# Optimization experiments

Hardware: AMD Instinct MI355X
Metric: run time of the kernel (lower is better)

The kernel has to match this reference:

```python
import jax, jax.numpy as jnp
import numpy as np

TOP_K = 50
TAU = 0.02
EPS = 1e-12  # torch F.normalize eps


def setup_inputs() -> dict:
    key = jax.random.key(0)
    k1, k2 = jax.random.split(key)
    test_patches = jax.random.normal(k1, (2048, 256), dtype=jnp.float32)
    memory_nodes_gpu = jax.random.normal(k2, (100000, 256), dtype=jnp.float32)
    return {"test_patches": test_patches, "memory_nodes_gpu": memory_nodes_gpu}


def _l2norm(x):
    n = jnp.linalg.norm(x, axis=-1, keepdims=True)
    return x / jnp.maximum(n, EPS)


def reference(test_patches, memory_nodes_gpu):
    # [P, M] similarity
    sim = jnp.matmul(test_patches, memory_nodes_gpu.T)
    K = min(TOP_K, memory_nodes_gpu.shape[0])
    topk_sim, topk_idx = jax.lax.top_k(sim, K)          # [P, K]
    attn = jax.nn.softmax(topk_sim / TAU, axis=1)        # [P, K]
    gathered = memory_nodes_gpu[topk_idx]                # [P, K, D]
    messages = jnp.einsum('pk,pkd->pd', attn, gathered)  # [P, D]
    updated = _l2norm(test_patches + messages)           # [P, D]
    evidence = topk_sim[:, 0]                            # [P]
    ew = jax.nn.softmax(evidence / TAU)[:, None]          # [P, 1]
    global_feature = jnp.sum(updated * ew, axis=0, keepdims=True)  # [1, D]
    return _l2norm(global_feature), updated
```

## Files before the change

kernel.cpp:

```cpp
#include <hip/hip_runtime.h>
#include <cstdint>
#include <cstddef>

#define NP      2048
#define NN      100000
#define DIM     256
#define NT      6250
#define NG      1563
#define NG2     3126
#define NG2R    3125
#define NGT2    3328
#define NTP     (NG * 4)
#define CPX     25
#define INV_TAU 50.0f
#define MARGIN  0.7f
#define CUT     0.553f
#define LCAP    64

typedef __fp16 half8  __attribute__((ext_vector_type(8)));
typedef __fp16 half2v __attribute__((ext_vector_type(2)));
typedef float  floatx4 __attribute__((ext_vector_type(4)));

union H8 { half8 v8; half2v v2[4]; };

typedef const __attribute__((address_space(1))) char* gptr_t;
typedef __attribute__((address_space(3))) char* sptr_t;

__device__ __forceinline__ unsigned enc_f32(float f) {
    unsigned b = __float_as_uint(f);
    return (b & 0x80000000u) ? ~b : (b | 0x80000000u);
}
__device__ __forceinline__ float dec_f32(unsigned u) {
    unsigned b = (u & 0x80000000u) ? (u & 0x7FFFFFFFu) : ~u;
    return __uint_as_float(b);
}

__global__ __launch_bounds__(512)
void k_convB(const float* __restrict__ B, __fp16* __restrict__ Bh,
             unsigned* __restrict__ me_u)
{
    const int t    = (int)blockIdx.x;
    const int ks   = (int)threadIdx.x >> 6;
    const int lane = (int)threadIdx.x & 63;
    if (t == 0 && threadIdx.x == 0) me_u[0] = 0u;
    H8 h;
    if (t < NT) {
        const int node = t * 16 + (lane & 15);
        const int d0   = ((lane >> 4) << 3) + (ks << 5);
        const float* bp = B + (size_t)node * DIM + d0;
        float4 b0 = *reinterpret_cast<const float4*>(bp);
        float4 b1 = *reinterpret_cast<const float4*>(bp + 4);
        h.v2[0] = __builtin_amdgcn_cvt_pkrtz(b0.x, b0.y);
        h.v2[1] = __builtin_amdgcn_cvt_pkrtz(b0.z, b0.w);
        h.v2[2] = __builtin_amdgcn_cvt_pkrtz(b1.x, b1.y);
        h.v2[3] = __builtin_amdgcn_cvt_pkrtz(b1.z, b1.w);
    } else {
        h.v2[0] = __builtin_amdgcn_cvt_pkrtz(0.f, 0.f);
        h.v2[1] = h.v2[0]; h.v2[2] = h.v2[0]; h.v2[3] = h.v2[0];
    }
    *reinterpret_cast<half8*>(Bh + (((size_t)t * 8 + ks) * 64 + lane) * 8) = h.v8;
}

__global__ __launch_bounds__(256, 2)
void k_pass1(const float* __restrict__ A, const __fp16* __restrict__ Bh,
             float* __restrict__ tmax2)
{
    __shared__ __fp16 lds[2][16384];

    const int tid  = (int)threadIdx.x;
    const int w    = tid >> 6;
    const int lane = tid & 63;
    const int col  = lane & 15;
    const int kg   = lane >> 4;

    const int bid   = (int)blockIdx.x;
    const int chunk = (bid & 7) * 8 + ((bid >> 3) & 7);
    const int rb    = bid >> 6;

    const int g0 = chunk * CPX;
    if (g0 >= NG) return;
    const int g1 = (g0 + CPX < NG) ? g0 + CPX : NG;
    const int wrow0 = rb * 256 + w * 64;

    H8 af[4][8];
#pragma unroll
    for (int rs = 0; rs < 4; ++rs) {
        const float* ap = A + (size_t)(wrow0 + rs * 16 + col) * DIM + (kg << 3);
#pragma unroll
        for (int ks = 0; ks < 8; ++ks) {
            float4 x0 = *reinterpret_cast<const float4*>(ap + (ks << 5));
            float4 x1 = *reinterpret_cast<const float4*>(ap + (ks << 5) + 4);
            af[rs][ks].v2[0] = __builtin_amdgcn_cvt_pkrtz(x0.x, x0.y);
            af[rs][ks].v2[1] = __builtin_amdgcn_cvt_pkrtz(x0.z, x0.w);
            af[rs][ks].v2[2] = __builtin_amdgcn_cvt_pkrtz(x1.x, x1.y);
            af[rs][ks].v2[3] = __builtin_amdgcn_cvt_pkrtz(x1.z, x1.w);
        }
    }

    auto STAGE = [&](int buf, int g) {
        const char* src = (const char*)Bh + ((size_t)g << 15) + (w << 13) + (lane << 4);
        char* dstb = (char*)&lds[buf][0] + (w << 13);
#pragma unroll
        for (int i = 0; i < 8; ++i)
            __builtin_amdgcn_global_load_lds((gptr_t)(src + (i << 10)),
                                             (sptr_t)(dstb + (i << 10)), 16, 0, 0);
    };

    STAGE(0, g0);
    int cur = 0;
    for (int g = g0; g < g1; ++g) {
        asm volatile("s_waitcnt vmcnt(0)" ::: "memory");
        __syncthreads();
        if (g + 1 < g1) STAGE(cur ^ 1, g + 1);

        const __fp16* base = &lds[cur][0] + lane * 8;
        float tmh[2][4];
#pragma unroll
        for (int hh = 0; hh < 2; ++hh)
#pragma unroll
            for (int rs = 0; rs < 4; ++rs) tmh[hh][rs] = -INFINITY;

        half8 bfA[8], bfB[8];
#pragma unroll
        for (int ks = 0; ks < 8; ++ks)
            bfA[ks] = *reinterpret_cast<const half8*>(base + ks * 512);

        auto FMI = [&](half8 (&curf)[8], half8 (&nxtf)[8], int ttn, bool ld, int hh) {
            floatx4 acc[4];
#pragma unroll
            for (int rs = 0; rs < 4; ++rs) acc[rs] = (floatx4){0.f, 0.f, 0.f, 0.f};
#pragma unroll
            for (int ks = 0; ks < 8; ++ks) {
                if (ld)
                    nxtf[ks] = *reinterpret_cast<const half8*>(base + ttn * 4096 + ks * 512);
                acc[0] = __builtin_amdgcn_mfma_f32_16x16x32_f16(curf[ks], af[0][ks].v8, acc[0], 0, 0, 0);
                acc[1] = __builtin_amdgcn_mfma_f32_16x16x32_f16(curf[ks], af[1][ks].v8, acc[1], 0, 0, 0);
                acc[2] = __builtin_amdgcn_mfma_f32_16x16x32_f16(curf[ks], af[2][ks].v8, acc[2], 0, 0, 0);
                acc[3] = __builtin_amdgcn_mfma_f32_16x16x32_f16(curf[ks], af[3][ks].v8, acc[3], 0, 0, 0);
            }
#pragma unroll
            for (int rs = 0; rs < 4; ++rs)
                tmh[hh][rs] = fmaxf(tmh[hh][rs], fmaxf(fmaxf(acc[rs][0], acc[rs][1]),
                                                       fmaxf(acc[rs][2], acc[rs][3])));
        };

        FMI(bfA, bfB, 1, true,  0);
        FMI(bfB, bfA, 2, true,  0);
        FMI(bfA, bfB, 3, true,  1);
        FMI(bfB, bfA, 0, false, 1);

#pragma unroll
        for (int hh = 0; hh < 2; ++hh)
#pragma unroll
            for (int rs = 0; rs < 4; ++rs) {
                tmh[hh][rs] = fmaxf(tmh[hh][rs], __shfl_xor(tmh[hh][rs], 16));
                tmh[hh][rs] = fmaxf(tmh[hh][rs], __shfl_xor(tmh[hh][rs], 32));
            }
        if (kg == 0) {
#pragma unroll
            for (int hh = 0; hh < 2; ++hh)
#pragma unroll
                for (int rs = 0; rs < 4; ++rs)
                    tmax2[(size_t)(g * 2 + hh) * NP + wrow0 + rs * 16 + col] = tmh[hh][rs];
        }
        cur ^= 1;
    }
}

__global__ __launch_bounds__(256)
void k_tr(const float* __restrict__ tmax2, float* __restrict__ tmaxT)
{
    __shared__ float tile[64][65];
    const int t  = (int)threadIdx.x;
    const int g0 = (int)blockIdx.x * 64;
    const int r0 = (int)blockIdx.y * 64;
    const int a  = t & 63;
    const int b  = t >> 6;
#pragma unroll
    for (int it = 0; it < 16; ++it) {
        int gi = b + it * 4;
        int g  = g0 + gi;
        tile[gi][a] = (g < NG2) ? tmax2[(size_t)g * NP + r0 + a] : -INFINITY;
    }
    __syncthreads();
#pragma unroll
    for (int it = 0; it < 16; ++it) {
        int ri = b + it * 4;
        tmaxT[(size_t)(r0 + ri) * NGT2 + g0 + a] = tile[a][ri];
    }
}

__global__ __launch_bounds__(256)
void k_finish(const float* __restrict__ A, const float* __restrict__ B,
              const float* __restrict__ tmaxT, float* __restrict__ out,
              float* __restrict__ evidence, unsigned* __restrict__ me_u)
{
    __shared__ float ald8[8][36];
    __shared__ float sims[32];
    __shared__ float red[8];
    __shared__ int   list[LCAP];
    __shared__ int   wsum[4];

    const int t    = (int)threadIdx.x;
    const int row  = (int)blockIdx.x;
    const int lane = t & 63;
    const int wv   = t >> 6;

    const float av_own = A[(size_t)row * DIM + t];
    ald8[t >> 5][t & 31] = av_own;

    float v[13];
    const float* tr = tmaxT + (size_t)row * NGT2 + t * 13;
    float M = -INFINITY;
#pragma unroll
    for (int k = 0; k < 13; ++k) { v[k] = tr[k]; M = fmaxf(M, v[k]); }
#pragma unroll
    for (int o = 1; o < 64; o <<= 1) M = fmaxf(M, __shfl_xor(M, o));
    if (lane == 0) red[wv] = M;
    __syncthreads();
    M = fmaxf(fmaxf(red[0], red[1]), fmaxf(red[2], red[3]));

    const float thr = M - MARGIN;
    int cnt = 0; unsigned mask13 = 0u;
#pragma unroll
    for (int k = 0; k < 13; ++k)
        if (v[k] > thr && (t * 13 + k) < NG2R) { mask13 |= (1u << k); ++cnt; }
    int pre = cnt;
#pragma unroll
    for (int o = 1; o < 64; o <<= 1) {
        int x = __shfl_up(pre, o);
        if (lane >= o) pre += x;
    }
    if (lane == 63) wsum[wv] = pre;
    __syncthreads();
    int woff = 0;
    for (int i = 0; i < wv; ++i) woff += wsum[i];
    int pos = woff + pre - cnt;
    if (mask13) {
#pragma unroll
        for (int k = 0; k < 13; ++k)
            if (mask13 & (1u << k)) {
                if (pos < LCAP) list[pos] = t * 13 + k;
                ++pos;
            }
    }
    __syncthreads();
    int total = wsum[0] + wsum[1] + wsum[2] + wsum[3];
    if (total > LCAP) total = LCAP;

    float m = -INFINITY, l = 0.f, msg = 0.f;
    const int n = t >> 3, q8 = t & 7;

    for (int e = 0; e < total; ++e) {
        const int g  = list[e];
        const int n0 = g * 32;
        {
            float s = 0.f;
            const float4* bp = reinterpret_cast<const float4*>(B + (size_t)(n0 + n) * DIM + q8 * 32);
            const float4* ap = reinterpret_cast<const float4*>(&ald8[q8][0]);
#pragma unroll
            for (int i = 0; i < 8; ++i) {
                float4 b4 = bp[i], a4 = ap[i];
                s += a4.x * b4.x + a4.y * b4.y + a4.z * b4.z + a4.w * b4.w;
            }
            s += __shfl_xor(s, 1);
            s += __shfl_xor(s, 2);
            s += __shfl_xor(s, 4);
            __syncthreads();
            if (q8 == 0) sims[n] = s;
            __syncthreads();
        }
        float gm = -INFINITY;
#pragma unroll
        for (int i = 0; i < 32; ++i) gm = fmaxf(gm, sims[i]);
        if (gm > m) {
            float sc = __expf((m - gm) * INV_TAU);
            m = gm; l *= sc; msg *= sc;
        }
        const float cut = m - CUT;
        for (int i = 0; i < 32; ++i) {
            float si = sims[i];
            if (si > cut) {
                float wn = __expf((si - m) * INV_TAU);
                l += wn;
                msg += wn * B[(size_t)(n0 + i) * DIM + t];
            }
        }
    }

    float u = av_own + msg * (1.0f / l);
    float ss = u * u;
#pragma unroll
    for (int o = 1; o < 64; o <<= 1) ss += __shfl_xor(ss, o);
    if (lane == 0) red[4 + wv] = ss;
    __syncthreads();
    ss = (red[4] + red[5]) + (red[6] + red[7]);
    float rn = 1.0f / fmaxf(sqrtf(ss), 1e-12f);
    out[256 + (size_t)row * DIM + t] = u * rn;
    if (t == 0) {
        evidence[row] = m;
        atomicMax(me_u, enc_f32(m));
    }
}

__global__ __launch_bounds__(256)
void k_gpart(const float* __restrict__ evidence, const unsigned* __restrict__ me_u,
             const float* __restrict__ out, float* __restrict__ gpart)
{
    __shared__ float wsh[128];
    int tid = (int)threadIdx.x;
    int r0  = blockIdx.x * 128;
    float Me = dec_f32(me_u[0]);
    if (tid < 128) wsh[tid] = __expf((evidence[r0 + tid] - Me) * INV_TAU);
    __syncthreads();
    float g = 0.0f;
    for (int k = 0; k < 128; ++k)
        g += wsh[k] * out[256 + (size_t)(r0 + k) * DIM + tid];
    gpart[blockIdx.x * 256 + tid] = g;
}

__global__ __launch_bounds__(256)
void k_final(const float* __restrict__ gpart, float* __restrict__ out)
{
    __shared__ float red[256];
    int tid = (int)threadIdx.x;
    float g = 0.0f;
#pragma unroll
    for (int b = 0; b < 16; ++b) g += gpart[b * 256 + tid];
    red[tid] = g * g; __syncthreads();
    for (int s = 128; s > 0; s >>= 1) {
        if (tid < s) red[tid] += red[tid + s];
        __syncthreads();
    }
    float n = sqrtf(red[0]);
    float r = 1.0f / fmaxf(n, 1e-12f);
    out[tid] = g * r;
}

extern "C" void kernel_launch(void* const* d_in, const int* in_sizes, int n_in,
                              void* d_out, int out_size, void* d_ws, size_t ws_size,
                              hipStream_t stream)
{
    const float* A = (const float*)d_in[0];
    const float* B = (const float*)d_in[1];
    float* out = (float*)d_out;
    float* ws  = (float*)d_ws;

    __fp16* Bh      = (__fp16*)ws;
    float* tmaxT    = ws;
    float* tmax2    = ws + (size_t)NTP * 2048;
    float* evidence = tmax2 + (size_t)NG2 * NP;
    unsigned* me_u  = (unsigned*)(evidence + NP);
    float* gpart    = (float*)(me_u + 16);

    k_convB <<<NTP,           512, 0, stream>>>(B, Bh, me_u);
    k_pass1 <<<512,           256, 0, stream>>>(A, Bh, tmax2);
    k_tr    <<<dim3(52, 32),  256, 0, stream>>>(tmax2, tmaxT);
    k_finish<<<NP,            256, 0, stream>>>(A, B, tmaxT, out, evidence, me_u);
    k_gpart <<<16,            256, 0, stream>>>(evidence, me_u, out, gpart);
    k_final <<<1,             256, 0, stream>>>(gpart, out);
}
```

Before: 182.6 us.

## Load B fragments directly from global and write transposed tile maxima, dropping transpose kernel

k_pass1 no longer stages B tiles into LDS with global_load_lds and barriers. Each wave now reads its half8 fragments straight from global memory into registers, double-buffered across tile pairs. It writes the per-row group maxima directly in row-major tmaxT layout, so the separate k_tr transpose kernel and its tmax2 buffer are removed. k_finish masks out-of-range entries at load time instead of relying on -inf padding. This trades LDS sharing and coalesced stores for per-wave global reads, which depend on L2 hits, and for strided scattered stores of the maxima.

Result: slower. 186.4 us (+2.1%).

```diff
diff --git a/kernel.cpp b/kernel.cpp
--- a/kernel.cpp
+++ b/kernel.cpp
@@ -7,7 +7,6 @@
 #define DIM     256
 #define NT      6250
 #define NG      1563
-#define NG2     3126
 #define NG2R    3125
 #define NGT2    3328
 #define NTP     (NG * 4)
@@ -22,9 +21,6 @@
 typedef float  floatx4 __attribute__((ext_vector_type(4)));
 
 union H8 { half8 v8; half2v v2[4]; };
-
-typedef const __attribute__((address_space(1))) char* gptr_t;
-typedef __attribute__((address_space(3))) char* sptr_t;
 
 __device__ __forceinline__ unsigned enc_f32(float f) {
     unsigned b = __float_as_uint(f);
@@ -63,10 +59,8 @@
 
 __global__ __launch_bounds__(256, 2)
 void k_pass1(const float* __restrict__ A, const __fp16* __restrict__ Bh,
-             float* __restrict__ tmax2)
-{
-    __shared__ __fp16 lds[2][16384];
-
+             float* __restrict__ tmaxT)
+{
     const int tid  = (int)threadIdx.x;
     const int w    = tid >> 6;
     const int lane = tid & 63;
@@ -97,96 +91,53 @@
         }
     }
 
-    auto STAGE = [&](int buf, int g) {
-        const char* src = (const char*)Bh + ((size_t)g << 15) + (w << 13) + (lane << 4);
-        char* dstb = (char*)&lds[buf][0] + (w << 13);
-#pragma unroll
-        for (int i = 0; i < 8; ++i)
-            __builtin_amdgcn_global_load_lds((gptr_t)(src + (i << 10)),
-                                             (sptr_t)(dstb + (i << 10)), 16, 0, 0);
+    const half8* bbl = reinterpret_cast<const half8*>(Bh) + lane;
+
+    float tm[4];
+    auto LD = [&](half8 (&bf)[8], int tt) {
+#pragma unroll
+        for (int ks = 0; ks < 8; ++ks)
+            bf[ks] = bbl[(size_t)tt * 512 + ks * 64];
     };
-
-    STAGE(0, g0);
-    int cur = 0;
-    for (int g = g0; g < g1; ++g) {
-        asm volatile("s_waitcnt vmcnt(0)" ::: "memory");
-        __syncthreads();
-        if (g + 1 < g1) STAGE(cur ^ 1, g + 1);
-
-        const __fp16* base = &lds[cur][0] + lane * 8;
-        float tmh[2][4];
-#pragma unroll
-        for (int hh = 0; hh < 2; ++hh)
-#pragma unroll
-            for (int rs = 0; rs < 4; ++rs) tmh[hh][rs] = -INFINITY;
-
-        half8 bfA[8], bfB[8];
-#pragma unroll
-        for (int ks = 0; ks < 8; ++ks)
-            bfA[ks] = *reinterpret_cast<const half8*>(base + ks * 512);
-
-        auto FMI = [&](half8 (&curf)[8], half8 (&nxtf)[8], int ttn, bool ld, int hh) {
-            floatx4 acc[4];
-#pragma unroll
-            for (int rs = 0; rs < 4; ++rs) acc[rs] = (floatx4){0.f, 0.f, 0.f, 0.f};
-#pragma unroll
-            for (int ks = 0; ks < 8; ++ks) {
-                if (ld)
-                    nxtf[ks] = *reinterpret_cast<const half8*>(base + ttn * 4096 + ks * 512);
-                acc[0] = __builtin_amdgcn_mfma_f32_16x16x32_f16(curf[ks], af[0][ks].v8, acc[0], 0, 0, 0);
-                acc[1] = __builtin_amdgcn_mfma_f32_16x16x32_f16(curf[ks], af[1][ks].v8, acc[1], 0, 0, 0);
-                acc[2] = __builtin_amdgcn_mfma_f32_16x16x32_f16(curf[ks], af[2][ks].v8, acc[2], 0, 0, 0);
-                acc[3] = __builtin_amdgcn_mfma_f32_16x16x32_f16(curf[ks], af[3][ks].v8, acc[3], 0, 0, 0);
-            }
+    auto FM = [&](const half8 (&bf)[8]) {
+        floatx4 acc[4];
+#pragma unroll
+        for (int rs = 0; rs < 4; ++rs) acc[rs] = (floatx4){0.f, 0.f, 0.f, 0.f};
+#pragma unroll
+        for (int ks = 0; ks < 8; ++ks) {
+            acc[0] = __builtin_amdgcn_mfma_f32_16x16x32_f16(bf[ks], af[0][ks].v8, acc[0], 0, 0, 0);
+            acc[1] = __builtin_amdgcn_mfma_f32_16x16x32_f16(bf[ks], af[1][ks].v8, acc[1], 0, 0, 0);
+            acc[2] = __builtin_amdgcn_mfma_f32_16x16x32_f16(bf[ks], af[2][ks].v8, acc[2], 0, 0, 0);
+            acc[3] = __builtin_amdgcn_mfma_f32_16x16x32_f16(bf[ks], af[3][ks].v8, acc[3], 0, 0, 0);
+        }
+#pragma unroll
+        for (int rs = 0; rs < 4; ++rs)
+            tm[rs] = fmaxf(tm[rs], fmaxf(fmaxf(acc[rs][0], acc[rs][1]),
+                                         fmaxf(acc[rs][2], acc[rs][3])));
+    };
+
+    const int T0 = g0 * 4, T1 = g1 * 4;
+    half8 bf0[8], bf1[8];
+    LD(bf0, T0);
+    for (int t = T0; t < T1; t += 2) {
+        LD(bf1, t + 1);
+        tm[0] = -INFINITY; tm[1] = -INFINITY;
+        tm[2] = -INFINITY; tm[3] = -INFINITY;
+        FM(bf0);
+        if (t + 2 < T1) LD(bf0, t + 2);
+        FM(bf1);
+
+#pragma unroll
+        for (int rs = 0; rs < 4; ++rs) {
+            tm[rs] = fmaxf(tm[rs], __shfl_xor(tm[rs], 16));
+            tm[rs] = fmaxf(tm[rs], __shfl_xor(tm[rs], 32));
+        }
+        if (kg == 0) {
+            const int g2 = t >> 1;
 #pragma unroll
             for (int rs = 0; rs < 4; ++rs)
-                tmh[hh][rs] = fmaxf(tmh[hh][rs], fmaxf(fmaxf(acc[rs][0], acc[rs][1]),
-                                                       fmaxf(acc[rs][2], acc[rs][3])));
-        };
-
-        FMI(bfA, bfB, 1, true,  0);
-        FMI(bfB, bfA, 2, true,  0);
-        FMI(bfA, bfB, 3, true,  1);
-        FMI(bfB, bfA, 0, false, 1);
-
-#pragma unroll
-        for (int hh = 0; hh < 2; ++hh)
-#pragma unroll
-            for (int rs = 0; rs < 4; ++rs) {
-                tmh[hh][rs] = fmaxf(tmh[hh][rs], __shfl_xor(tmh[hh][rs], 16));
-                tmh[hh][rs] = fmaxf(tmh[hh][rs], __shfl_xor(tmh[hh][rs], 32));
-            }
-        if (kg == 0) {
-#pragma unroll
-            for (int hh = 0; hh < 2; ++hh)
-#pragma unroll
-                for (int rs = 0; rs < 4; ++rs)
-                    tmax2[(size_t)(g * 2 + hh) * NP + wrow0 + rs * 16 + col] = tmh[hh][rs];
-        }
-        cur ^= 1;
-    }
-}
-
-__global__ __launch_bounds__(256)
-void k_tr(const float* __restrict__ tmax2, float* __restrict__ tmaxT)
-{
-    __shared__ float tile[64][65];
-    const int t  = (int)threadIdx.x;
-    const int g0 = (int)blockIdx.x * 64;
-    const int r0 = (int)blockIdx.y * 64;
-    const int a  = t & 63;
-    const int b  = t >> 6;
-#pragma unroll
-    for (int it = 0; it < 16; ++it) {
-        int gi = b + it * 4;
-        int g  = g0 + gi;
-        tile[gi][a] = (g < NG2) ? tmax2[(size_t)g * NP + r0 + a] : -INFINITY;
-    }
-    __syncthreads();
-#pragma unroll
-    for (int it = 0; it < 16; ++it) {
-        int ri = b + it * 4;
-        tmaxT[(size_t)(r0 + ri) * NGT2 + g0 + a] = tile[a][ri];
+                tmaxT[(size_t)(wrow0 + rs * 16 + col) * NGT2 + g2] = tm[rs];
+        }
     }
 }
 
@@ -213,7 +164,10 @@
     const float* tr = tmaxT + (size_t)row * NGT2 + t * 13;
     float M = -INFINITY;
 #pragma unroll
-    for (int k = 0; k < 13; ++k) { v[k] = tr[k]; M = fmaxf(M, v[k]); }
+    for (int k = 0; k < 13; ++k) {
+        v[k] = (t * 13 + k < NG2R) ? tr[k] : -INFINITY;
+        M = fmaxf(M, v[k]);
+    }
 #pragma unroll
     for (int o = 1; o < 64; o <<= 1) M = fmaxf(M, __shfl_xor(M, o));
     if (lane == 0) red[wv] = M;
@@ -224,7 +178,7 @@
     int cnt = 0; unsigned mask13 = 0u;
 #pragma unroll
     for (int k = 0; k < 13; ++k)
-        if (v[k] > thr && (t * 13 + k) < NG2R) { mask13 |= (1u << k); ++cnt; }
+        if (v[k] > thr) { mask13 |= (1u << k); ++cnt; }
     int pre = cnt;
 #pragma unroll
     for (int o = 1; o < 64; o <<= 1) {
@@ -347,16 +301,14 @@
     float* ws  = (float*)d_ws;
 
     __fp16* Bh      = (__fp16*)ws;
-    float* tmaxT    = ws;
-    float* tmax2    = ws + (size_t)NTP * 2048;
-    float* evidence = tmax2 + (size_t)NG2 * NP;
+    float* tmaxT    = ws + (size_t)NTP * 2048;
+    float* evidence = tmaxT + (size_t)NP * NGT2;
     unsigned* me_u  = (unsigned*)(evidence + NP);
     float* gpart    = (float*)(me_u + 16);
 
-    k_convB <<<NTP,           512, 0, stream>>>(B, Bh, me_u);
-    k_pass1 <<<512,           256, 0, stream>>>(A, Bh, tmax2);
-    k_tr    <<<dim3(52, 32),  256, 0, stream>>>(tmax2, tmaxT);
-    k_finish<<<NP,            256, 0, stream>>>(A, B, tmaxT, out, evidence, me_u);
-    k_gpart <<<16,            256, 0, stream>>>(evidence, me_u, out, gpart);
-    k_final <<<1,             256, 0, stream>>>(gpart, out);
-}
+    k_convB <<<NTP, 512, 0, stream>>>(B, Bh, me_u);
+    k_pass1 <<<512, 256, 0, stream>>>(A, Bh, tmaxT);
+    k_finish<<<NP,  256, 0, stream>>>(A, B, tmaxT, out, evidence, me_u);
+    k_gpart <<<16,  256, 0, stream>>>(evidence, me_u, out, gpart);
+    k_final <<<1,   256, 0, stream>>>(gpart, out);
+}
```

## Use four-deep half-size LDS pipeline with partial vmcnt waits in pass1

Applied to the files above, without the earlier changes.

The k_pass1 staging loop moves from double-buffered 32KB groups (4 tiles) to a 4-slot ring of 16KB subgroups (2 tiles). Three loads are kept in flight, and each step waits with a partial vmcnt count, so global-to-LDS copies overlap more with the MFMA work. __syncthreads is replaced by a raw s_barrier. Each iteration now does less work per barrier, and correctness depends on the hand-set vmcnt counts matching the issued loads.

After: 188.0 us. 2.9% more time.

```diff
diff --git a/kernel.cpp b/kernel.cpp
--- a/kernel.cpp
+++ b/kernel.cpp
@@ -6,12 +6,11 @@
 #define NN      100000
 #define DIM     256
 #define NT      6250
-#define NG      1563
 #define NG2     3126
 #define NG2R    3125
 #define NGT2    3328
-#define NTP     (NG * 4)
-#define CPX     25
+#define NTP     (NG2 * 2)
+#define SGPC    50
 #define INV_TAU 50.0f
 #define MARGIN  0.7f
 #define CUT     0.553f
@@ -65,7 +64,7 @@
 void k_pass1(const float* __restrict__ A, const __fp16* __restrict__ Bh,
              float* __restrict__ tmax2)
 {
-    __shared__ __fp16 lds[2][16384];
+    __shared__ __fp16 lds[4][8192];
 
     const int tid  = (int)threadIdx.x;
     const int w    = tid >> 6;
@@ -77,9 +76,9 @@
     const int chunk = (bid & 7) * 8 + ((bid >> 3) & 7);
     const int rb    = bid >> 6;
 
-    const int g0 = chunk * CPX;
-    if (g0 >= NG) return;
-    const int g1 = (g0 + CPX < NG) ? g0 + CPX : NG;
+    const int s0 = chunk * SGPC;
+    if (s0 >= NG2) return;
+    const int s1 = (s0 + SGPC < NG2) ? s0 + SGPC : NG2;
     const int wrow0 = rb * 256 + w * 64;
 
     H8 af[4][8];
@@ -97,73 +96,78 @@
         }
     }
 
-    auto STAGE = [&](int buf, int g) {
-        const char* src = (const char*)Bh + ((size_t)g << 15) + (w << 13) + (lane << 4);
-        char* dstb = (char*)&lds[buf][0] + (w << 13);
-#pragma unroll
-        for (int i = 0; i < 8; ++i)
+    auto STAGE = [&](int buf, int sg) {
+        const char* src = (const char*)Bh + ((size_t)sg << 14) + (w << 12) + (lane << 4);
+        char* dstb = (char*)&lds[buf][0] + (w << 12);
+#pragma unroll
+        for (int i = 0; i < 4; ++i)
             __builtin_amdgcn_global_load_lds((gptr_t)(src + (i << 10)),
                                              (sptr_t)(dstb + (i << 10)), 16, 0, 0);
     };
 
-    STAGE(0, g0);
-    int cur = 0;
-    for (int g = g0; g < g1; ++g) {
-        asm volatile("s_waitcnt vmcnt(0)" ::: "memory");
-        __syncthreads();
-        if (g + 1 < g1) STAGE(cur ^ 1, g + 1);
-
-        const __fp16* base = &lds[cur][0] + lane * 8;
-        float tmh[2][4];
-#pragma unroll
-        for (int hh = 0; hh < 2; ++hh)
-#pragma unroll
-            for (int rs = 0; rs < 4; ++rs) tmh[hh][rs] = -INFINITY;
+    STAGE(0, s0);
+    if (s0 + 1 < s1) STAGE(1, s0 + 1);
+    if (s0 + 2 < s1) STAGE(2, s0 + 2);
+
+    for (int sg = s0; sg < s1; ++sg) {
+        if (sg <= s1 - 3)      asm volatile("s_waitcnt vmcnt(8)" ::: "memory");
+        else if (sg == s1 - 2) asm volatile("s_waitcnt vmcnt(4)" ::: "memory");
+        else                   asm volatile("s_waitcnt vmcnt(0)" ::: "memory");
+        asm volatile("s_barrier" ::: "memory");
+        if (sg + 3 < s1) STAGE((sg + 3 - s0) & 3, sg + 3);
+
+        const __fp16* base = &lds[(sg - s0) & 3][0] + lane * 8;
+        float tm[4] = { -INFINITY, -INFINITY, -INFINITY, -INFINITY };
 
         half8 bfA[8], bfB[8];
 #pragma unroll
         for (int ks = 0; ks < 8; ++ks)
             bfA[ks] = *reinterpret_cast<const half8*>(base + ks * 512);
 
-        auto FMI = [&](half8 (&curf)[8], half8 (&nxtf)[8], int ttn, bool ld, int hh) {
+        {
             floatx4 acc[4];
 #pragma unroll
             for (int rs = 0; rs < 4; ++rs) acc[rs] = (floatx4){0.f, 0.f, 0.f, 0.f};
 #pragma unroll
             for (int ks = 0; ks < 8; ++ks) {
-                if (ld)
-                    nxtf[ks] = *reinterpret_cast<const half8*>(base + ttn * 4096 + ks * 512);
-                acc[0] = __builtin_amdgcn_mfma_f32_16x16x32_f16(curf[ks], af[0][ks].v8, acc[0], 0, 0, 0);
-                acc[1] = __builtin_amdgcn_mfma_f32_16x16x32_f16(curf[ks], af[1][ks].v8, acc[1], 0, 0, 0);
-                acc[2] = __builtin_amdgcn_mfma_f32_16x16x32_f16(curf[ks], af[2][ks].v8, acc[2], 0, 0, 0);
-                acc[3] = __builtin_amdgcn_mfma_f32_16x16x32_f16(curf[ks], af[3][ks].v8, acc[3], 0, 0, 0);
+                bfB[ks] = *reinterpret_cast<const half8*>(base + 4096 + ks * 512);
+                acc[0] = __builtin_amdgcn_mfma_f32_16x16x32_f16(bfA[ks], af[0][ks].v8, acc[0], 0, 0, 0);
+                acc[1] = __builtin_amdgcn_mfma_f32_16x16x32_f16(bfA[ks], af[1][ks].v8, acc[1], 0, 0, 0);
+                acc[2] = __builtin_amdgcn_mfma_f32_16x16x32_f16(bfA[ks], af[2][ks].v8, acc[2], 0, 0, 0);
+                acc[3] = __builtin_amdgcn_mfma_f32_16x16x32_f16(bfA[ks], af[3][ks].v8, acc[3], 0, 0, 0);
             }
 #pragma unroll
             for (int rs = 0; rs < 4; ++rs)
-                tmh[hh][rs] = fmaxf(tmh[hh][rs], fmaxf(fmaxf(acc[rs][0], acc[rs][1]),
-                                                       fmaxf(acc[rs][2], acc[rs][3])));
-        };
-
-        FMI(bfA, bfB, 1, true,  0);
-        FMI(bfB, bfA, 2, true,  0);
-        FMI(bfA, bfB, 3, true,  1);
-        FMI(bfB, bfA, 0, false, 1);
-
-#pragma unroll
-        for (int hh = 0; hh < 2; ++hh)
-#pragma unroll
-            for (int rs = 0; rs < 4; ++rs) {
-                tmh[hh][rs] = fmaxf(tmh[hh][rs], __shfl_xor(tmh[hh][rs], 16));
-                tmh[hh][rs] = fmaxf(tmh[hh][rs], __shfl_xor(tmh[hh][rs], 32));
-            }
+                tm[rs] = fmaxf(tm[rs], fmaxf(fmaxf(acc[rs][0], acc[rs][1]),
+                                             fmaxf(acc[rs][2], acc[rs][3])));
+        }
+        {
+            floatx4 acc[4];
+#pragma unroll
+            for (int rs = 0; rs < 4; ++rs) acc[rs] = (floatx4){0.f, 0.f, 0.f, 0.f};
+#pragma unroll
+            for (int ks = 0; ks < 8; ++ks) {
+                acc[0] = __builtin_amdgcn_mfma_f32_16x16x32_f16(bfB[ks], af[0][ks].v8, acc[0], 0, 0, 0);
+                acc[1] = __builtin_amdgcn_mfma_f32_16x16x32_f16(bfB[ks], af[1][ks].v8, acc[1], 0, 0, 0);
+                acc[2] = __builtin_amdgcn_mfma_f32_16x16x32_f16(bfB[ks], af[2][ks].v8, acc[2], 0, 0, 0);
+                acc[3] = __builtin_amdgcn_mfma_f32_16x16x32_f16(bfB[ks], af[3][ks].v8, acc[3], 0, 0, 0);
+            }
+#pragma unroll
+            for (int rs = 0; rs < 4; ++rs)
+                tm[rs] = fmaxf(tm[rs], fmaxf(fmaxf(acc[rs][0], acc[rs][1]),
+                                             fmaxf(acc[rs][2], acc[rs][3])));
+        }
+
+#pragma unroll
+        for (int rs = 0; rs < 4; ++rs) {
+            tm[rs] = fmaxf(tm[rs], __shfl_xor(tm[rs], 16));
+            tm[rs] = fmaxf(tm[rs], __shfl_xor(tm[rs], 32));
+        }
         if (kg == 0) {
 #pragma unroll
-            for (int hh = 0; hh < 2; ++hh)
-#pragma unroll
-                for (int rs = 0; rs < 4; ++rs)
-                    tmax2[(size_t)(g * 2 + hh) * NP + wrow0 + rs * 16 + col] = tmh[hh][rs];
-        }
-        cur ^= 1;
+            for (int rs = 0; rs < 4; ++rs)
+                tmax2[(size_t)sg * NP + wrow0 + rs * 16 + col] = tm[rs];
+        }
     }
 }
 
```
